# Kernel tuning notes

Measured on AMD Instinct MI355X. Metric: run time of the kernel, lower is better.

Reference implementation:

```python
import jax, jax.numpy as jnp
import numpy as np

NBINS = 256

def _equalize_channel(img):
    # img: [H, W] int32 in [0, 255]
    flat = img.reshape(-1)
    histo = jax.ops.segment_sum(jnp.ones_like(flat), flat, num_segments=NBINS)  # [256] int32
    # last nonzero bin count (tf: nonzero_histo[-1])
    mask = histo != 0
    last_idx = (NBINS - 1) - jnp.argmax(mask[::-1])
    last_nonzero = histo[last_idx]
    # sum of nonzero histo == sum of histo (zeros contribute nothing)
    step = (jnp.sum(histo) - last_nonzero) // 255
    safe_step = jnp.maximum(step, 1)  # avoid div-by-zero; result unused when step==0
    lut = (jnp.cumsum(histo) + safe_step // 2) // safe_step
    lut = jnp.concatenate([jnp.zeros((1,), histo.dtype), lut[:-1]])
    lut = jnp.clip(lut, 0, 255)
    out = jnp.where(step == 0, img, lut[flat].reshape(img.shape))
    return out.astype(jnp.uint8)


def setup_inputs() -> dict:
    key = jax.random.key(0)
    images = jax.random.randint(key, (64, 512, 512, 3), 0, 256, dtype=jnp.int32)
    return {"images": images}


def reference(images):
    # images: [B, H, W, 3] int32 in [0, 255]
    # per-image, per-channel histogram equalization
    chw = jnp.transpose(images, (0, 3, 1, 2))  # [B, 3, H, W]
    eq = jax.vmap(jax.vmap(_equalize_channel))(chw)  # [B, 3, H, W] uint8
    return jnp.transpose(eq, (0, 2, 3, 1))  # [B, H, W, 3]
```

## Files before the change

kernel.cpp:

```cpp
#include <hip/hip_runtime.h>

constexpr int NBINS = 256;
constexpr int HPI = 3 * NBINS;
constexpr int BPI = 24;

typedef int iv4 __attribute__((ext_vector_type(4)));

__global__ __launch_bounds__(256)
void hist_part_kernel(const iv4* __restrict__ in, int* __restrict__ part,
                      unsigned* __restrict__ packed, int n4_per_img) {
    __shared__ int subh[4][HPI];
    const int tid = threadIdx.x;
    const int wave = tid >> 6;

    for (int i = tid; i < 4 * HPI; i += 256) ((int*)subh)[i] = 0;
    __syncthreads();

    const int img = blockIdx.x / BPI;
    const int blk = blockIdx.x % BPI;
    const size_t ibase = (size_t)img * n4_per_img;
    const iv4* p = in + ibase;
    unsigned* pk = packed + ibase;
    const int stride = BPI * 256;

    int i = blk * 256 + tid;
    int c0 = i % 3;
    int c1 = c0 + 1; if (c1 == 3) c1 = 0;
    int c2 = c1 + 1; if (c2 == 3) c2 = 0;
    int c3 = c2 + 1; if (c3 == 3) c3 = 0;
    const int b0 = c0 * NBINS, b1 = c1 * NBINS, b2 = c2 * NBINS, b3 = c3 * NBINS;

    for (; i + stride < n4_per_img; i += 2 * stride) {
        iv4 v0 = p[i];
        iv4 v1 = p[i + stride];
        pk[i]          = (unsigned)(v0.x & 255) | ((unsigned)(v0.y & 255) << 8) |
                         ((unsigned)(v0.z & 255) << 16) | ((unsigned)(v0.w & 255) << 24);
        pk[i + stride] = (unsigned)(v1.x & 255) | ((unsigned)(v1.y & 255) << 8) |
                         ((unsigned)(v1.z & 255) << 16) | ((unsigned)(v1.w & 255) << 24);
        atomicAdd(&subh[wave][b0 + (v0.x & 255)], 1);
        atomicAdd(&subh[wave][b1 + (v0.y & 255)], 1);
        atomicAdd(&subh[wave][b2 + (v0.z & 255)], 1);
        atomicAdd(&subh[wave][b3 + (v0.w & 255)], 1);
        atomicAdd(&subh[wave][b0 + (v1.x & 255)], 1);
        atomicAdd(&subh[wave][b1 + (v1.y & 255)], 1);
        atomicAdd(&subh[wave][b2 + (v1.z & 255)], 1);
        atomicAdd(&subh[wave][b3 + (v1.w & 255)], 1);
    }
    if (i < n4_per_img) {
        iv4 v = p[i];
        pk[i] = (unsigned)(v.x & 255) | ((unsigned)(v.y & 255) << 8) |
                ((unsigned)(v.z & 255) << 16) | ((unsigned)(v.w & 255) << 24);
        atomicAdd(&subh[wave][b0 + (v.x & 255)], 1);
        atomicAdd(&subh[wave][b1 + (v.y & 255)], 1);
        atomicAdd(&subh[wave][b2 + (v.z & 255)], 1);
        atomicAdd(&subh[wave][b3 + (v.w & 255)], 1);
    }
    __syncthreads();

    int* gp = part + (size_t)blockIdx.x * HPI;
    for (int e = tid; e < HPI; e += 256)
        gp[e] = subh[0][e] + subh[1][e] + subh[2][e] + subh[3][e];
}

__global__ __launch_bounds__(256)
void lut_kernel(const int* __restrict__ part, int* __restrict__ lut) {
    __shared__ int cum[NBINS];
    __shared__ int lastNZ;
    const int t = threadIdx.x;
    const int img = blockIdx.x / 3;
    const int ch  = blockIdx.x % 3;

    const int* p = part + (size_t)img * BPI * HPI + ch * NBINS + t;
    int h = 0;
    for (int b = 0; b < BPI; ++b) h += p[(size_t)b * HPI];

    cum[t] = h;
    if (t == 0) lastNZ = 0;
    __syncthreads();
    if (h > 0) atomicMax(&lastNZ, t);

    for (int off = 1; off < NBINS; off <<= 1) {
        int add = (t >= off) ? cum[t - off] : 0;
        __syncthreads();
        cum[t] += add;
        __syncthreads();
    }

    const int sum  = cum[NBINS - 1];
    const int last = lastNZ;
    const int hl   = cum[last] - (last > 0 ? cum[last - 1] : 0);
    const int step = (sum - hl) / 255;

    int v;
    if (step == 0) {
        v = t;
    } else {
        const int cp = (t == 0) ? 0 : cum[t - 1];
        v = (cp + (step >> 1)) / step;
        if (v > 255) v = 255;
    }
    lut[blockIdx.x * NBINS + t] = v;
}

__global__ __launch_bounds__(256)
void apply_kernel(const unsigned* __restrict__ packed, iv4* __restrict__ out,
                  const int* __restrict__ lut, int n4_per_img) {
    __shared__ int l[HPI];
    const int tid = threadIdx.x;
    const int img = blockIdx.x / BPI;
    const int blk = blockIdx.x % BPI;

    const int* gl = lut + (size_t)img * HPI;
    for (int i = tid; i < HPI; i += 256) l[i] = gl[i];
    __syncthreads();

    const size_t ibase = (size_t)img * n4_per_img;
    const unsigned* pk = packed + ibase;
    iv4* q = out + ibase;
    const int stride = BPI * 256;

    int i = blk * 256 + tid;
    int c0 = i % 3;
    int c1 = c0 + 1; if (c1 == 3) c1 = 0;
    int c2 = c1 + 1; if (c2 == 3) c2 = 0;
    int c3 = c2 + 1; if (c3 == 3) c3 = 0;
    const int b0 = c0 * NBINS, b1 = c1 * NBINS, b2 = c2 * NBINS, b3 = c3 * NBINS;

    for (; i + stride < n4_per_img; i += 2 * stride) {
        unsigned w0 = pk[i];
        unsigned w1 = pk[i + stride];
        iv4 o0, o1;
        o0.x = l[b0 + (w0 & 255)];
        o0.y = l[b1 + ((w0 >> 8) & 255)];
        o0.z = l[b2 + ((w0 >> 16) & 255)];
        o0.w = l[b3 + (w0 >> 24)];
        o1.x = l[b0 + (w1 & 255)];
        o1.y = l[b1 + ((w1 >> 8) & 255)];
        o1.z = l[b2 + ((w1 >> 16) & 255)];
        o1.w = l[b3 + (w1 >> 24)];
        __builtin_nontemporal_store(o0, &q[i]);
        __builtin_nontemporal_store(o1, &q[i + stride]);
    }
    if (i < n4_per_img) {
        unsigned w = pk[i];
        iv4 o;
        o.x = l[b0 + (w & 255)];
        o.y = l[b1 + ((w >> 8) & 255)];
        o.z = l[b2 + ((w >> 16) & 255)];
        o.w = l[b3 + (w >> 24)];
        __builtin_nontemporal_store(o, &q[i]);
    }
}

extern "C" void kernel_launch(void* const* d_in, const int* in_sizes, int n_in,
                              void* d_out, int out_size, void* d_ws, size_t ws_size,
                              hipStream_t stream) {
    const int* in = (const int*)d_in[0];
    int* out = (int*)d_out;

    const int npix = 512 * 512;
    const int ints_per_img = 3 * npix;
    const int n4_per_img = ints_per_img / 4;
    const int n_img = in_sizes[0] / ints_per_img;

    int* part = (int*)d_ws;
    int* lut  = part + (size_t)n_img * BPI * HPI;
    unsigned* packed = (unsigned*)(lut + (size_t)n_img * HPI);

    hist_part_kernel<<<n_img * BPI, 256, 0, stream>>>((const iv4*)in, part, packed, n4_per_img);
    lut_kernel<<<n_img * 3, 256, 0, stream>>>(part, lut);
    apply_kernel<<<n_img * BPI, 256, 0, stream>>>(packed, (iv4*)out, lut, n4_per_img);
}
```

Baseline: 86.67 us.

## Fuse LUT computation into apply kernel and use nontemporal input loads

Result: slower. 100.9 us (+16.4%).

```diff
diff --git a/kernel.cpp b/kernel.cpp
--- a/kernel.cpp
+++ b/kernel.cpp
@@ -31,8 +31,8 @@
     const int b0 = c0 * NBINS, b1 = c1 * NBINS, b2 = c2 * NBINS, b3 = c3 * NBINS;
 
     for (; i + stride < n4_per_img; i += 2 * stride) {
-        iv4 v0 = p[i];
-        iv4 v1 = p[i + stride];
+        iv4 v0 = __builtin_nontemporal_load(&p[i]);
+        iv4 v1 = __builtin_nontemporal_load(&p[i + stride]);
         pk[i]          = (unsigned)(v0.x & 255) | ((unsigned)(v0.y & 255) << 8) |
                          ((unsigned)(v0.z & 255) << 16) | ((unsigned)(v0.w & 255) << 24);
         pk[i + stride] = (unsigned)(v1.x & 255) | ((unsigned)(v1.y & 255) << 8) |
@@ -47,7 +47,7 @@
         atomicAdd(&subh[wave][b3 + (v1.w & 255)], 1);
     }
     if (i < n4_per_img) {
-        iv4 v = p[i];
+        iv4 v = __builtin_nontemporal_load(&p[i]);
         pk[i] = (unsigned)(v.x & 255) | ((unsigned)(v.y & 255) << 8) |
                 ((unsigned)(v.z & 255) << 16) | ((unsigned)(v.w & 255) << 24);
         atomicAdd(&subh[wave][b0 + (v.x & 255)], 1);
@@ -63,56 +63,56 @@
 }
 
 __global__ __launch_bounds__(256)
-void lut_kernel(const int* __restrict__ part, int* __restrict__ lut) {
+void lut_apply_kernel(const unsigned* __restrict__ packed, iv4* __restrict__ out,
+                      const int* __restrict__ part, int n4_per_img) {
     __shared__ int cum[NBINS];
+    __shared__ int lutS[HPI];
     __shared__ int lastNZ;
-    const int t = threadIdx.x;
-    const int img = blockIdx.x / 3;
-    const int ch  = blockIdx.x % 3;
 
-    const int* p = part + (size_t)img * BPI * HPI + ch * NBINS + t;
-    int h = 0;
-    for (int b = 0; b < BPI; ++b) h += p[(size_t)b * HPI];
-
-    cum[t] = h;
-    if (t == 0) lastNZ = 0;
-    __syncthreads();
-    if (h > 0) atomicMax(&lastNZ, t);
-
-    for (int off = 1; off < NBINS; off <<= 1) {
-        int add = (t >= off) ? cum[t - off] : 0;
-        __syncthreads();
-        cum[t] += add;
-        __syncthreads();
-    }
-
-    const int sum  = cum[NBINS - 1];
-    const int last = lastNZ;
-    const int hl   = cum[last] - (last > 0 ? cum[last - 1] : 0);
-    const int step = (sum - hl) / 255;
-
-    int v;
-    if (step == 0) {
-        v = t;
-    } else {
-        const int cp = (t == 0) ? 0 : cum[t - 1];
-        v = (cp + (step >> 1)) / step;
-        if (v > 255) v = 255;
-    }
-    lut[blockIdx.x * NBINS + t] = v;
-}
-
-__global__ __launch_bounds__(256)
-void apply_kernel(const unsigned* __restrict__ packed, iv4* __restrict__ out,
-                  const int* __restrict__ lut, int n4_per_img) {
-    __shared__ int l[HPI];
     const int tid = threadIdx.x;
     const int img = blockIdx.x / BPI;
     const int blk = blockIdx.x % BPI;
 
-    const int* gl = lut + (size_t)img * HPI;
-    for (int i = tid; i < HPI; i += 256) l[i] = gl[i];
-    __syncthreads();
+    const int* pp = part + (size_t)img * BPI * HPI;
+    int h[3];
+    #pragma unroll
+    for (int ch = 0; ch < 3; ++ch) {
+        int s = 0;
+        #pragma unroll 4
+        for (int b = 0; b < BPI; ++b) s += pp[b * HPI + ch * NBINS + tid];
+        h[ch] = s;
+    }
+
+    #pragma unroll
+    for (int ch = 0; ch < 3; ++ch) {
+        if (tid == 0) lastNZ = 0;
+        cum[tid] = h[ch];
+        __syncthreads();
+        if (h[ch] > 0) atomicMax(&lastNZ, tid);
+
+        for (int off = 1; off < NBINS; off <<= 1) {
+            int add = (tid >= off) ? cum[tid - off] : 0;
+            __syncthreads();
+            cum[tid] += add;
+            __syncthreads();
+        }
+
+        const int sum  = cum[NBINS - 1];
+        const int last = lastNZ;
+        const int hl   = cum[last] - (last > 0 ? cum[last - 1] : 0);
+        const int step = (sum - hl) / 255;
+
+        int v;
+        if (step == 0) {
+            v = tid;
+        } else {
+            const int cp = (tid == 0) ? 0 : cum[tid - 1];
+            v = (cp + (step >> 1)) / step;
+            if (v > 255) v = 255;
+        }
+        lutS[ch * NBINS + tid] = v;
+        __syncthreads();
+    }
 
     const size_t ibase = (size_t)img * n4_per_img;
     const unsigned* pk = packed + ibase;
@@ -130,24 +130,24 @@
         unsigned w0 = pk[i];
         unsigned w1 = pk[i + stride];
         iv4 o0, o1;
-        o0.x = l[b0 + (w0 & 255)];
-        o0.y = l[b1 + ((w0 >> 8) & 255)];
-        o0.z = l[b2 + ((w0 >> 16) & 255)];
-        o0.w = l[b3 + (w0 >> 24)];
-        o1.x = l[b0 + (w1 & 255)];
-        o1.y = l[b1 + ((w1 >> 8) & 255)];
-        o1.z = l[b2 + ((w1 >> 16) & 255)];
-        o1.w = l[b3 + (w1 >> 24)];
+        o0.x = lutS[b0 + (w0 & 255)];
+        o0.y = lutS[b1 + ((w0 >> 8) & 255)];
+        o0.z = lutS[b2 + ((w0 >> 16) & 255)];
+        o0.w = lutS[b3 + (w0 >> 24)];
+        o1.x = lutS[b0 + (w1 & 255)];
+        o1.y = lutS[b1 + ((w1 >> 8) & 255)];
+        o1.z = lutS[b2 + ((w1 >> 16) & 255)];
+        o1.w = lutS[b3 + (w1 >> 24)];
         __builtin_nontemporal_store(o0, &q[i]);
         __builtin_nontemporal_store(o1, &q[i + stride]);
     }
     if (i < n4_per_img) {
         unsigned w = pk[i];
         iv4 o;
-        o.x = l[b0 + (w & 255)];
-        o.y = l[b1 + ((w >> 8) & 255)];
-        o.z = l[b2 + ((w >> 16) & 255)];
-        o.w = l[b3 + (w >> 24)];
+        o.x = lutS[b0 + (w & 255)];
+        o.y = lutS[b1 + ((w >> 8) & 255)];
+        o.z = lutS[b2 + ((w >> 16) & 255)];
+        o.w = lutS[b3 + (w >> 24)];
         __builtin_nontemporal_store(o, &q[i]);
     }
 }
@@ -164,10 +164,8 @@
     const int n_img = in_sizes[0] / ints_per_img;
 
     int* part = (int*)d_ws;
-    int* lut  = part + (size_t)n_img * BPI * HPI;
-    unsigned* packed = (unsigned*)(lut + (size_t)n_img * HPI);
+    unsigned* packed = (unsigned*)(part + (size_t)n_img * BPI * HPI);
 
     hist_part_kernel<<<n_img * BPI, 256, 0, stream>>>((const iv4*)in, part, packed, n4_per_img);
-    lut_kernel<<<n_img * 3, 256, 0, stream>>>(part, lut);
-    apply_kernel<<<n_img * BPI, 256, 0, stream>>>(packed, (iv4*)out, lut, n4_per_img);
+    lut_apply_kernel<<<n_img * BPI, 256, 0, stream>>>(packed, (iv4*)out, part, n4_per_img);
 }
```
